# Optimization experiments

Measured on AMD Instinct MI355X. Metric: run time of the kernel, lower is better.

The kernel has to match this reference:

```python
import jax, jax.numpy as jnp
import numpy as np

LAMBDA = 150.0


def setup_inputs() -> dict:
    key = jax.random.key(0)
    k1, k2 = jax.random.split(key)
    gru_outputs = jax.random.normal(k1, (8192, 4096), dtype=jnp.float32)
    target = jax.random.normal(k2, (8192, 4096), dtype=jnp.float32)
    return {"gru_outputs": gru_outputs, "target": target}


def reference(gru_outputs, target):
    # L1Loss with default 'mean' reduction
    l1_loss = jnp.mean(jnp.abs(gru_outputs - target))
    # smooth_loss: for each element hr_t of gru_outputs[:6].flatten(),
    # MyLoss.forward returns |hr_t - mean(hr_outs)|; summed then divided by T
    # => mean(|x - mean(x)|), computed in one fused pass instead of a python loop.
    x = gru_outputs[:6].reshape(-1)
    smooth = jnp.mean(jnp.abs(x - jnp.mean(x)))
    return l1_loss + LAMBDA * smooth
```

## Files before the change

### kernel.cpp

```cpp
#include <hip/hip_runtime.h>


#define N_TOTAL  (8192 * 4096)
#define N_SMOOTH (6 * 4096)
#define LAMBDA_F 150.0f

constexpr int BLOCKS  = 2048;
constexpr int THREADS = 256;
constexpr int N4           = N_TOTAL / 4;
constexpr int F4_PER_BLOCK = N4 / BLOCKS;
constexpr int ITERS        = F4_PER_BLOCK / THREADS;
constexpr int FT = 1024;

template <int NT>
__device__ __forceinline__ float block_reduce_bcast(float v) {
    __shared__ float ws[NT / 64 + 1];
    __syncthreads();
    #pragma unroll
    for (int off = 32; off > 0; off >>= 1) v += __shfl_down(v, off, 64);
    const int lane = threadIdx.x & 63;
    const int wid  = threadIdx.x >> 6;
    if (lane == 0) ws[wid] = v;
    __syncthreads();
    if (threadIdx.x == 0) {
        float s = 0.0f;
        #pragma unroll
        for (int w = 0; w < NT / 64; ++w) s += ws[w];
        ws[NT / 64] = s;
    }
    __syncthreads();
    return ws[NT / 64];
}

__device__ __forceinline__ float abs4(float4 va, float4 vb) {
    return fabsf(va.x - vb.x) + fabsf(va.y - vb.y) +
           fabsf(va.z - vb.z) + fabsf(va.w - vb.w);
}

__global__ __launch_bounds__(THREADS) void l1_partial_kernel(
    const float4* __restrict__ a, const float4* __restrict__ b,
    float* __restrict__ partial) {
    const int base = blockIdx.x * F4_PER_BLOCK + threadIdx.x;
    float s0 = 0.0f, s1 = 0.0f, s2 = 0.0f, s3 = 0.0f;
    #pragma unroll
    for (int g = 0; g < ITERS / 4; ++g) {
        const int i0 = base + (g * 4 + 0) * THREADS;
        const int i1 = base + (g * 4 + 1) * THREADS;
        const int i2 = base + (g * 4 + 2) * THREADS;
        const int i3 = base + (g * 4 + 3) * THREADS;
        float4 a0 = a[i0]; float4 a1 = a[i1]; float4 a2 = a[i2]; float4 a3 = a[i3];
        float4 b0 = b[i0]; float4 b1 = b[i1]; float4 b2 = b[i2]; float4 b3 = b[i3];
        s0 += abs4(a0, b0);
        s1 += abs4(a1, b1);
        s2 += abs4(a2, b2);
        s3 += abs4(a3, b3);
    }
    float bs = block_reduce_bcast<THREADS>((s0 + s1) + (s2 + s3));
    if (threadIdx.x == 0) partial[blockIdx.x] = bs;
}

__global__ __launch_bounds__(FT) void finalize_kernel(
    const float* __restrict__ partial, const float* __restrict__ gru,
    float* __restrict__ out) {
    float s = 0.0f;
    #pragma unroll
    for (int i = threadIdx.x; i < BLOCKS; i += FT) s += partial[i];
    float l1_sum = block_reduce_bcast<FT>(s);

    const float4* x4 = (const float4*)gru;
    constexpr int NS4 = N_SMOOTH / 4;
    float xs = 0.0f;
    #pragma unroll
    for (int i = threadIdx.x; i < NS4; i += FT) {
        float4 v = x4[i];
        xs += (v.x + v.y) + (v.z + v.w);
    }
    float x_mean = block_reduce_bcast<FT>(xs) / (float)N_SMOOTH;

    float ds = 0.0f;
    #pragma unroll
    for (int i = threadIdx.x; i < NS4; i += FT) {
        float4 v = x4[i];
        ds += fabsf(v.x - x_mean) + fabsf(v.y - x_mean) +
              fabsf(v.z - x_mean) + fabsf(v.w - x_mean);
    }
    float dev_sum = block_reduce_bcast<FT>(ds);

    if (threadIdx.x == 0) {
        out[0] = l1_sum / (float)N_TOTAL + LAMBDA_F * (dev_sum / (float)N_SMOOTH);
    }
}

extern "C" void kernel_launch(void* const* d_in, const int* in_sizes, int n_in,
                              void* d_out, int out_size, void* d_ws, size_t ws_size,
                              hipStream_t stream) {
    const float* gru = (const float*)d_in[0];
    const float* tgt = (const float*)d_in[1];
    float* out     = (float*)d_out;
    float* partial = (float*)d_ws;

    l1_partial_kernel<<<BLOCKS, THREADS, 0, stream>>>(
        (const float4*)gru, (const float4*)tgt, partial);
    finalize_kernel<<<1, FT, 0, stream>>>(partial, gru, out);
}
```

Before: 48.19 us.

## Move smooth-loss reduction into main kernel's extra block, use nontemporal loads

Adds one extra block to the L1 partial kernel that computes the smooth-loss mean and deviation sum, so the single-block finalize kernel no longer serially reads the first 6 rows twice. The first 768 blocks use nontemporal loads, presumably to limit cache pollution so the smooth-block and later reads hit cache. The finalize kernel shrinks to 256 threads with vectorized partial reads. The extra block runs serially on one CU and could become a tail if it is scheduled late.

```diff
diff --git a/kernel.cpp b/kernel.cpp
--- a/kernel.cpp
+++ b/kernel.cpp
@@ -10,7 +10,9 @@
 constexpr int N4           = N_TOTAL / 4;
 constexpr int F4_PER_BLOCK = N4 / BLOCKS;
 constexpr int ITERS        = F4_PER_BLOCK / THREADS;
-constexpr int FT = 1024;
+constexpr int NT_BLOCKS = 768;
+
+typedef float vf4 __attribute__((ext_vector_type(4)));
 
 template <int NT>
 __device__ __forceinline__ float block_reduce_bcast(float v) {
@@ -32,14 +34,20 @@
     return ws[NT / 64];
 }
 
-__device__ __forceinline__ float abs4(float4 va, float4 vb) {
+__device__ __forceinline__ float abs4(vf4 va, vf4 vb) {
     return fabsf(va.x - vb.x) + fabsf(va.y - vb.y) +
            fabsf(va.z - vb.z) + fabsf(va.w - vb.w);
 }
 
-__global__ __launch_bounds__(THREADS) void l1_partial_kernel(
-    const float4* __restrict__ a, const float4* __restrict__ b,
-    float* __restrict__ partial) {
+template <bool NTLOAD>
+__device__ __forceinline__ vf4 ld4(const vf4* p) {
+    if constexpr (NTLOAD) return __builtin_nontemporal_load(p);
+    else                  return *p;
+}
+
+template <bool NTLOAD>
+__device__ __forceinline__ float l1_chunk(const vf4* __restrict__ a,
+                                          const vf4* __restrict__ b) {
     const int base = blockIdx.x * F4_PER_BLOCK + threadIdx.x;
     float s0 = 0.0f, s1 = 0.0f, s2 = 0.0f, s3 = 0.0f;
     #pragma unroll
@@ -48,45 +56,57 @@
         const int i1 = base + (g * 4 + 1) * THREADS;
         const int i2 = base + (g * 4 + 2) * THREADS;
         const int i3 = base + (g * 4 + 3) * THREADS;
-        float4 a0 = a[i0]; float4 a1 = a[i1]; float4 a2 = a[i2]; float4 a3 = a[i3];
-        float4 b0 = b[i0]; float4 b1 = b[i1]; float4 b2 = b[i2]; float4 b3 = b[i3];
+        vf4 a0 = ld4<NTLOAD>(a + i0); vf4 a1 = ld4<NTLOAD>(a + i1);
+        vf4 a2 = ld4<NTLOAD>(a + i2); vf4 a3 = ld4<NTLOAD>(a + i3);
+        vf4 b0 = ld4<NTLOAD>(b + i0); vf4 b1 = ld4<NTLOAD>(b + i1);
+        vf4 b2 = ld4<NTLOAD>(b + i2); vf4 b3 = ld4<NTLOAD>(b + i3);
         s0 += abs4(a0, b0);
         s1 += abs4(a1, b1);
         s2 += abs4(a2, b2);
         s3 += abs4(a3, b3);
     }
-    float bs = block_reduce_bcast<THREADS>((s0 + s1) + (s2 + s3));
-    if (threadIdx.x == 0) partial[blockIdx.x] = bs;
+    return (s0 + s1) + (s2 + s3);
 }
 
-__global__ __launch_bounds__(FT) void finalize_kernel(
-    const float* __restrict__ partial, const float* __restrict__ gru,
-    float* __restrict__ out) {
+__global__ __launch_bounds__(THREADS) void l1_partial_kernel(
+    const vf4* __restrict__ a, const vf4* __restrict__ b,
+    float* __restrict__ partial) {
+    if (blockIdx.x < BLOCKS) {
+        float s = (blockIdx.x < NT_BLOCKS) ? l1_chunk<true>(a, b)
+                                           : l1_chunk<false>(a, b);
+        float bs = block_reduce_bcast<THREADS>(s);
+        if (threadIdx.x == 0) partial[blockIdx.x] = bs;
+    } else {
+        constexpr int NS4 = N_SMOOTH / 4;
+        float xs = 0.0f;
+        for (int i = threadIdx.x; i < NS4; i += THREADS) {
+            vf4 v = a[i];
+            xs += (v.x + v.y) + (v.z + v.w);
+        }
+        float x_mean = block_reduce_bcast<THREADS>(xs) / (float)N_SMOOTH;
+        float ds = 0.0f;
+        for (int i = threadIdx.x; i < NS4; i += THREADS) {
+            vf4 v = a[i];
+            ds += fabsf(v.x - x_mean) + fabsf(v.y - x_mean) +
+                  fabsf(v.z - x_mean) + fabsf(v.w - x_mean);
+        }
+        float dev_sum = block_reduce_bcast<THREADS>(ds);
+        if (threadIdx.x == 0) partial[BLOCKS] = dev_sum;
+    }
+}
+
+__global__ __launch_bounds__(THREADS) void finalize_kernel(
+    const float* __restrict__ partial, float* __restrict__ out) {
+    const vf4* p4 = (const vf4*)partial;
     float s = 0.0f;
     #pragma unroll
-    for (int i = threadIdx.x; i < BLOCKS; i += FT) s += partial[i];
-    float l1_sum = block_reduce_bcast<FT>(s);
-
-    const float4* x4 = (const float4*)gru;
-    constexpr int NS4 = N_SMOOTH / 4;
-    float xs = 0.0f;
-    #pragma unroll
-    for (int i = threadIdx.x; i < NS4; i += FT) {
-        float4 v = x4[i];
-        xs += (v.x + v.y) + (v.z + v.w);
+    for (int i = threadIdx.x; i < BLOCKS / 4; i += THREADS) {
+        vf4 v = p4[i];
+        s += (v.x + v.y) + (v.z + v.w);
     }
-    float x_mean = block_reduce_bcast<FT>(xs) / (float)N_SMOOTH;
-
-    float ds = 0.0f;
-    #pragma unroll
-    for (int i = threadIdx.x; i < NS4; i += FT) {
-        float4 v = x4[i];
-        ds += fabsf(v.x - x_mean) + fabsf(v.y - x_mean) +
-              fabsf(v.z - x_mean) + fabsf(v.w - x_mean);
-    }
-    float dev_sum = block_reduce_bcast<FT>(ds);
-
+    float l1_sum = block_reduce_bcast<THREADS>(s);
     if (threadIdx.x == 0) {
+        float dev_sum = partial[BLOCKS];
         out[0] = l1_sum / (float)N_TOTAL + LAMBDA_F * (dev_sum / (float)N_SMOOTH);
     }
 }
@@ -99,7 +119,7 @@
     float* out     = (float*)d_out;
     float* partial = (float*)d_ws;
 
-    l1_partial_kernel<<<BLOCKS, THREADS, 0, stream>>>(
-        (const float4*)gru, (const float4*)tgt, partial);
-    finalize_kernel<<<1, FT, 0, stream>>>(partial, gru, out);
+    l1_partial_kernel<<<BLOCKS + 1, THREADS, 0, stream>>>(
+        (const vf4*)gru, (const vf4*)tgt, partial);
+    finalize_kernel<<<1, THREADS, 0, stream>>>(partial, out);
 }
```

Measured after the change: 48.29 us. About the same (+0.2%).
